# Optimization experiments

Hardware: AMD Instinct MI355X
Metric: run time of the kernel (lower is better)

The kernel has to match this reference:

```python
import jax, jax.numpy as jnp
import numpy as np

H = 128
N_GENE = 100000
N_VAR = 200000
E = 500000


def setup_inputs() -> dict:
    key = jax.random.key(0)
    ks = jax.random.split(key, 24)
    s = 0.05
    inp = {
        "emb_gene": jax.random.normal(ks[0], (N_GENE, H), jnp.float32) * s,
        "emb_var": jax.random.normal(ks[1], (N_VAR, H), jnp.float32) * s,
        "Wl1_gv": jax.random.normal(ks[2], (H, H), jnp.float32) * s,
        "bl1_gv": jnp.zeros((H,), jnp.float32),
        "Wr1_gv": jax.random.normal(ks[3], (H, H), jnp.float32) * s,
        "Wl1_vg": jax.random.normal(ks[4], (H, H), jnp.float32) * s,
        "bl1_vg": jnp.zeros((H,), jnp.float32),
        "Wr1_vg": jax.random.normal(ks[5], (H, H), jnp.float32) * s,
        "Wl2_gv": jax.random.normal(ks[6], (H, H), jnp.float32) * s,
        "bl2_gv": jnp.zeros((H,), jnp.float32),
        "Wr2_gv": jax.random.normal(ks[7], (H, H), jnp.float32) * s,
        "Wl2_vg": jax.random.normal(ks[8], (H, H), jnp.float32) * s,
        "bl2_vg": jnp.zeros((H,), jnp.float32),
        "Wr2_vg": jax.random.normal(ks[9], (H, H), jnp.float32) * s,
        "A1": jax.random.normal(ks[10], (H, H), jnp.float32) * s,
        "b1": jnp.zeros((H,), jnp.float32),
        "A2": jax.random.normal(ks[11], (8, H), jnp.float32) * s,
        "b2": jnp.zeros((8,), jnp.float32),
        "src_gv": jax.random.randint(ks[12], (E,), 0, N_GENE, jnp.int32),
        "dst_gv": jax.random.randint(ks[13], (E,), 0, N_VAR, jnp.int32),
        "src_vg": jax.random.randint(ks[14], (E,), 0, N_VAR, jnp.int32),
        "dst_vg": jax.random.randint(ks[15], (E,), 0, N_GENE, jnp.int32),
    }
    return inp


def _sage(x_src, x_dst, src, dst, Wl, bl, Wr):
    # PyG SAGEConv: lin_l(mean_{j->i} x_src[j]) + lin_r(x_dst[i])
    msg = x_src[src]                                             # [E, H] gather
    agg = jax.ops.segment_sum(msg, dst, num_segments=x_dst.shape[0])
    cnt = jax.ops.segment_sum(jnp.ones_like(src, x_src.dtype), dst,
                              num_segments=x_dst.shape[0])
    mean = agg / jnp.maximum(cnt, 1.0)[:, None]
    return mean @ Wl.T + bl + x_dst @ Wr.T


def reference(emb_gene, emb_var,
              Wl1_gv, bl1_gv, Wr1_gv, Wl1_vg, bl1_vg, Wr1_vg,
              Wl2_gv, bl2_gv, Wr2_gv, Wl2_vg, bl2_vg, Wr2_vg,
              A1, b1, A2, b2,
              src_gv, dst_gv, src_vg, dst_vg):
    # layer 1: gene->variant updates variant; variant->gene updates gene
    h_var = _sage(emb_gene, emb_var, src_gv, dst_gv, Wl1_gv, bl1_gv, Wr1_gv)
    h_gene = _sage(emb_var, emb_gene, src_vg, dst_vg, Wl1_vg, bl1_vg, Wr1_vg)
    z_gene = jax.nn.relu(h_gene)
    z_var = jax.nn.relu(h_var)
    # layer 2
    z_var2 = _sage(z_gene, z_var, src_gv, dst_gv, Wl2_gv, bl2_gv, Wr2_gv)
    z_gene2 = _sage(z_var, z_gene, src_vg, dst_vg, Wl2_vg, bl2_vg, Wr2_vg)
    # adversarial head on 'gene' (GradReverse is identity in forward)
    hdn = jax.nn.relu(z_gene2 @ A1.T + b1)
    adv_gene = hdn @ A2.T + b2
    return (z_gene2, z_var2, adv_gene)
```

## Files before the change

kernel.cpp:

```cpp
#include <hip/hip_runtime.h>
#include <hip/hip_bf16.h>

typedef unsigned short u16;
typedef unsigned int u32;
typedef __attribute__((ext_vector_type(8))) short bf16x8;
typedef __attribute__((ext_vector_type(4))) float f32x4;

#define NG 100000
#define NV 200000
#define NE 500000
#define HD 128
#define NALL (NG + NV)
#define EALL (2 * NE)

__device__ __forceinline__ float bflo(u32 w) { return __uint_as_float(w << 16); }
__device__ __forceinline__ float bfhi(u32 w) { return __uint_as_float(w & 0xffff0000u); }
__device__ __forceinline__ u16 f2bf(float f) {
    __hip_bfloat16 h = __float2bfloat16(f);
    u16 u; __builtin_memcpy(&u, &h, 2); return u;
}
__device__ __forceinline__ u32 pk2(float a, float b) {
    return (u32)f2bf(a) | ((u32)f2bf(b) << 16);
}

__global__ __launch_bounds__(256) void cvt_kernel(const float* __restrict__ g,
                                                  const float* __restrict__ v,
                                                  u16* __restrict__ out) {
    size_t slot = (size_t)blockIdx.x * 256 + threadIdx.x;
    size_t off = slot * 8;
    if (off >= (size_t)NALL * HD) return;
    const float* p = (off < (size_t)NG * HD) ? (g + off) : (v + (off - (size_t)NG * HD));
    float4 a = *(const float4*)p;
    float4 b = *(const float4*)(p + 4);
    uint4 pk;
    pk.x = pk2(a.x, a.y); pk.y = pk2(a.z, a.w);
    pk.z = pk2(b.x, b.y); pk.w = pk2(b.z, b.w);
    *(uint4*)(out + off) = pk;
}

__global__ __launch_bounds__(256) void wcvt_kernel(
    const float* w0, const float* w1, const float* w2, const float* w3,
    const float* w4, const float* w5, const float* w6, const float* w7,
    const float* w8, u16* __restrict__ out)
{
    const float* Ws[9] = {w0, w1, w2, w3, w4, w5, w6, w7, w8};
    const float* W = Ws[blockIdx.x];
    u16* o = out + (size_t)blockIdx.x * 16384;
    int tid = threadIdx.x;
#pragma unroll
    for (int it = 0; it < 8; ++it) {
        int slot = it * 256 + tid;
        int f = slot >> 6, l = slot & 63;
        int kt = f >> 3, ct = f & 7;
        int row = ct * 16 + (l & 15);
        int kof = kt * 32 + (l >> 4) * 8;
        const float* wp = W + (size_t)row * HD + kof;
        float4 x = *(const float4*)wp;
        float4 y = *(const float4*)(wp + 4);
        uint4 pk;
        pk.x = pk2(x.x, x.y); pk.y = pk2(x.z, x.w);
        pk.z = pk2(y.x, y.y); pk.w = pk2(y.z, y.w);
        *(uint4*)(o + (size_t)slot * 8) = pk;
    }
}

__global__ __launch_bounds__(256) void hist2_kernel(const int* __restrict__ dst_gv,
                                                    const int* __restrict__ dst_vg,
                                                    int* __restrict__ deg) {
    int t = blockIdx.x * 256 + threadIdx.x;
    if (t < NE)            atomicAdd(&deg[dst_gv[t]], 1);
    else if (t < EALL)     atomicAdd(&deg[NV + dst_vg[t - NE]], 1);
}

__global__ __launch_bounds__(256) void scan1_kernel(const int* __restrict__ deg,
                                                    int* __restrict__ excl,
                                                    int* __restrict__ bsum, int N) {
    __shared__ int lds[256];
    int tid = threadIdx.x;
    int base = blockIdx.x * 2048 + tid * 8;
    int v[8]; int s = 0;
#pragma unroll
    for (int i = 0; i < 8; ++i) { v[i] = (base + i < N) ? deg[base + i] : 0; s += v[i]; }
    lds[tid] = s;
    __syncthreads();
    for (int off = 1; off < 256; off <<= 1) {
        int x = (tid >= off) ? lds[tid - off] : 0;
        __syncthreads();
        lds[tid] += x;
        __syncthreads();
    }
    int run = lds[tid] - s;
#pragma unroll
    for (int i = 0; i < 8; ++i) {
        if (base + i < N) excl[base + i] = run;
        run += v[i];
    }
    if (tid == 255) bsum[blockIdx.x] = lds[255];
}

__global__ void scan2_kernel(int* __restrict__ bsum, int nb) {
    if (threadIdx.x == 0 && blockIdx.x == 0) {
        int run = 0;
        for (int i = 0; i < nb; ++i) { int t = bsum[i]; bsum[i] = run; run += t; }
    }
}

__global__ __launch_bounds__(256) void scan3_kernel(int* __restrict__ rs,
                                                    int* __restrict__ cur,
                                                    const int* __restrict__ bsum, int N) {
    int i = blockIdx.x * 256 + threadIdx.x;
    if (i < N) {
        int v = rs[i] + bsum[i >> 11];
        rs[i] = v;
        cur[i] = v;
    }
    if (i == 0) rs[N] = EALL;
}

__global__ __launch_bounds__(256) void escatter2_kernel(const int* __restrict__ src_gv,
                                                        const int* __restrict__ dst_gv,
                                                        const int* __restrict__ src_vg,
                                                        const int* __restrict__ dst_vg,
                                                        int* __restrict__ cur,
                                                        int* __restrict__ esrc) {
    int t = blockIdx.x * 256 + threadIdx.x;
    if (t < NE) {
        int p = atomicAdd(&cur[dst_gv[t]], 1);
        esrc[p] = src_gv[t];
    } else if (t < EALL) {
        int e = t - NE;
        int p = atomicAdd(&cur[NV + dst_vg[e]], 1);
        esrc[p] = NG + src_vg[e];
    }
}

template <int RELU, int OBF16>
__global__ __launch_bounds__(256, 4) void fused_sage_kernel(
    const u16* __restrict__ Xb,
    const int* __restrict__ rs,
    const int* __restrict__ esrc,
    const u16* __restrict__ wf_v, const u16* __restrict__ wf_g,
    const float* __restrict__ b_v, const float* __restrict__ b_g,
    float* __restrict__ outf_v, float* __restrict__ outf_g,
    u16* __restrict__ outb_v, u16* __restrict__ outb_g,
    int nvb)
{
    __shared__ __align__(16) char ldsbuf[33792];
    u16* atile = (u16*)ldsbuf;

    const bool isVar = (int)blockIdx.x < nvb;
    const int bseg = isVar ? blockIdx.x : blockIdx.x - nvb;
    const int Nseg = isVar ? NV : NG;
    const int gseg = isVar ? 0 : NV;
    const u16* Xseg = Xb + (size_t)(isVar ? NG : 0) * HD;
    const u16* wf = isVar ? wf_v : wf_g;
    const float* bias = isVar ? b_v : b_g;
    float* outf = isVar ? outf_v : outf_g;
    u16* outb = isVar ? outb_v : outb_g;

    const int tid = threadIdx.x;
    const int lane = tid & 63;
    const int wid = tid >> 6;
    const int m0 = bseg * 128 + wid * 32;
    const int lr = lane & 15, lg = lane >> 4;

    {
        const int c = tid & 15;
        for (int it = 0; it < 8; ++it) {
            int lrow = it * 16 + (tid >> 4);
            int srow = bseg * 128 + lrow;
            float s[8] = {0.f, 0.f, 0.f, 0.f, 0.f, 0.f, 0.f, 0.f};
            float rcv = 0.f;
            if (srow < Nseg) {
                int e0 = rs[gseg + srow], e1 = rs[gseg + srow + 1];
                int e = e0;
                for (; e + 2 <= e1; e += 2) {
                    const u16* p0 = Xb + (size_t)esrc[e] * HD + c * 8;
                    const u16* p1 = Xb + (size_t)esrc[e + 1] * HD + c * 8;
                    uint4 u0 = *(const uint4*)p0;
                    uint4 u1 = *(const uint4*)p1;
                    u32 w0[4] = {u0.x, u0.y, u0.z, u0.w};
                    u32 w1[4] = {u1.x, u1.y, u1.z, u1.w};
#pragma unroll
                    for (int i = 0; i < 4; ++i) {
                        s[2 * i] += bflo(w0[i]) + bflo(w1[i]);
                        s[2 * i + 1] += bfhi(w0[i]) + bfhi(w1[i]);
                    }
                }
                if (e < e1) {
                    const u16* p = Xb + (size_t)esrc[e] * HD + c * 8;
                    uint4 u = *(const uint4*)p;
                    u32 w[4] = {u.x, u.y, u.z, u.w};
#pragma unroll
                    for (int i = 0; i < 4; ++i) { s[2 * i] += bflo(w[i]); s[2 * i + 1] += bfhi(w[i]); }
                }
                rcv = 1.f / fmaxf((float)(e1 - e0), 1.f);
            }
            uint4 pk;
            pk.x = pk2(s[0] * rcv, s[1] * rcv);
            pk.y = pk2(s[2] * rcv, s[3] * rcv);
            pk.z = pk2(s[4] * rcv, s[5] * rcv);
            pk.w = pk2(s[6] * rcv, s[7] * rcv);
            *(uint4*)(atile + lrow * 128 + ((c ^ (lrow & 15)) << 3)) = pk;
        }
    }
    __syncthreads();

    f32x4 acc[2][8];
#pragma unroll
    for (int rt = 0; rt < 2; ++rt)
#pragma unroll
        for (int ct = 0; ct < 8; ++ct) acc[rt][ct] = (f32x4){0.f, 0.f, 0.f, 0.f};

    {
        const u16* wp = wf;
        bf16x8 a[4][2];
#pragma unroll
        for (int kt = 0; kt < 4; ++kt)
#pragma unroll
            for (int rt = 0; rt < 2; ++rt) {
                int lrow = wid * 32 + rt * 16 + lr;
                int ck = (kt * 4 + lg) ^ (lrow & 15);
                a[kt][rt] = *(const bf16x8*)(atile + lrow * 128 + (ck << 3));
            }
#pragma unroll
        for (int kt = 0; kt < 4; ++kt)
#pragma unroll
            for (int ct = 0; ct < 8; ++ct) {
                bf16x8 w = *(const bf16x8*)(wp + (size_t)(((kt * 8 + ct) << 6) + lane) * 8);
#pragma unroll
                for (int rt = 0; rt < 2; ++rt)
                    acc[rt][ct] = __builtin_amdgcn_mfma_f32_16x16x32_bf16(
                        a[kt][rt], w, acc[rt][ct], 0, 0, 0);
            }
    }
    {
        const u16* wp = wf + 16384;
        bf16x8 a[4][2];
#pragma unroll
        for (int kt = 0; kt < 4; ++kt)
#pragma unroll
            for (int rt = 0; rt < 2; ++rt) {
                int row = m0 + rt * 16 + lr; if (row > Nseg - 1) row = Nseg - 1;
                a[kt][rt] = *(const bf16x8*)(Xseg + (size_t)row * HD + kt * 32 + lg * 8);
            }
#pragma unroll
        for (int kt = 0; kt < 4; ++kt)
#pragma unroll
            for (int ct = 0; ct < 8; ++ct) {
                bf16x8 w = *(const bf16x8*)(wp + (size_t)(((kt * 8 + ct) << 6) + lane) * 8);
#pragma unroll
                for (int rt = 0; rt < 2; ++rt)
                    acc[rt][ct] = __builtin_amdgcn_mfma_f32_16x16x32_bf16(
                        a[kt][rt], w, acc[rt][ct], 0, 0, 0);
            }
    }

    float bv[8];
#pragma unroll
    for (int ct = 0; ct < 8; ++ct) bv[ct] = bias[ct * 16 + lr];

    __syncthreads();
    float (*lds_t)[16][132] = (float (*)[16][132])ldsbuf;
#pragma unroll
    for (int rt = 0; rt < 2; ++rt) {
#pragma unroll
        for (int ct = 0; ct < 8; ++ct)
#pragma unroll
            for (int r = 0; r < 4; ++r) {
                float v = acc[rt][ct][r] + bv[ct];
                if (RELU) v = fmaxf(v, 0.f);
                lds_t[wid][lg * 4 + r][ct * 16 + lr] = v;
            }
        __syncthreads();
        if (OBF16 == 0) {
#pragma unroll
            for (int i = 0; i < 8; ++i) {
                int row16 = i * 2 + (lane >> 5);
                int colb = (lane & 31) * 4;
                f32x4 v = *(const f32x4*)&lds_t[wid][row16][colb];
                int grow = m0 + rt * 16 + row16;
                if (grow < Nseg) *(f32x4*)(outf + (size_t)grow * HD + colb) = v;
            }
        } else {
#pragma unroll
            for (int i = 0; i < 4; ++i) {
                int row16 = i * 4 + (lane >> 4);
                int colb = (lane & 15) * 8;
                f32x4 v0 = *(const f32x4*)&lds_t[wid][row16][colb];
                f32x4 v1 = *(const f32x4*)&lds_t[wid][row16][colb + 4];
                uint4 pk;
                pk.x = pk2(v0[0], v0[1]); pk.y = pk2(v0[2], v0[3]);
                pk.z = pk2(v1[0], v1[1]); pk.w = pk2(v1[2], v1[3]);
                int grow = m0 + rt * 16 + row16;
                if (grow < Nseg) *(uint4*)(outb + (size_t)grow * HD + colb) = pk;
            }
        }
        __syncthreads();
    }
}

__global__ __launch_bounds__(256, 4) void head_kernel(
    const float* __restrict__ g2,
    const u16* __restrict__ wfA1,
    const float* __restrict__ b1,
    const float* __restrict__ A2,
    const float* __restrict__ b2,
    float* __restrict__ adv)
{
    __shared__ __align__(16) u16 lds_h[4][16][136];
    const int tid = threadIdx.x;
    const int lane = tid & 63;
    const int wid = tid >> 6;
    const int m0 = blockIdx.x * 128 + wid * 32;
    const int lr = lane & 15, lg = lane >> 4;

    bf16x8 a2f[4];
#pragma unroll
    for (int kt = 0; kt < 4; ++kt) {
        union { u16 s[8]; bf16x8 v; } u;
        if (lr < 8) {
            const float* p = A2 + (size_t)lr * HD + kt * 32 + lg * 8;
            float4 x = *(const float4*)p;
            float4 y = *(const float4*)(p + 4);
            u.s[0] = f2bf(x.x); u.s[1] = f2bf(x.y); u.s[2] = f2bf(x.z); u.s[3] = f2bf(x.w);
            u.s[4] = f2bf(y.x); u.s[5] = f2bf(y.y); u.s[6] = f2bf(y.z); u.s[7] = f2bf(y.w);
        } else {
#pragma unroll
            for (int i = 0; i < 8; ++i) u.s[i] = 0;
        }
        a2f[kt] = u.v;
    }

    f32x4 acc[2][8];
#pragma unroll
    for (int rt = 0; rt < 2; ++rt)
#pragma unroll
        for (int ct = 0; ct < 8; ++ct) acc[rt][ct] = (f32x4){0.f, 0.f, 0.f, 0.f};

#pragma unroll
    for (int kt = 0; kt < 4; ++kt) {
        bf16x8 a[2];
#pragma unroll
        for (int rt = 0; rt < 2; ++rt) {
            int row = m0 + rt * 16 + lr; if (row > NG - 1) row = NG - 1;
            const float* p = g2 + (size_t)row * HD + kt * 32 + lg * 8;
            float4 x = *(const float4*)p;
            float4 y = *(const float4*)(p + 4);
            union { u16 s[8]; bf16x8 v; } u;
            u.s[0] = f2bf(x.x); u.s[1] = f2bf(x.y); u.s[2] = f2bf(x.z); u.s[3] = f2bf(x.w);
            u.s[4] = f2bf(y.x); u.s[5] = f2bf(y.y); u.s[6] = f2bf(y.z); u.s[7] = f2bf(y.w);
            a[rt] = u.v;
        }
#pragma unroll
        for (int ct = 0; ct < 8; ++ct) {
            bf16x8 w = *(const bf16x8*)(wfA1 + (size_t)(((kt * 8 + ct) << 6) + lane) * 8);
#pragma unroll
            for (int rt = 0; rt < 2; ++rt)
                acc[rt][ct] = __builtin_amdgcn_mfma_f32_16x16x32_bf16(
                    a[rt], w, acc[rt][ct], 0, 0, 0);
        }
    }

    float b1v[8];
#pragma unroll
    for (int ct = 0; ct < 8; ++ct) b1v[ct] = b1[ct * 16 + lr];
    float b2v = (lr < 8) ? b2[lr] : 0.f;

#pragma unroll
    for (int rt = 0; rt < 2; ++rt) {
#pragma unroll
        for (int ct = 0; ct < 8; ++ct)
#pragma unroll
            for (int r = 0; r < 4; ++r) {
                float v = fmaxf(acc[rt][ct][r] + b1v[ct], 0.f);
                lds_h[wid][lg * 4 + r][ct * 16 + lr] = f2bf(v);
            }
        __syncthreads();
        f32x4 av = (f32x4){0.f, 0.f, 0.f, 0.f};
#pragma unroll
        for (int kt = 0; kt < 4; ++kt) {
            bf16x8 h = *(const bf16x8*)&lds_h[wid][lr][kt * 32 + lg * 8];
            av = __builtin_amdgcn_mfma_f32_16x16x32_bf16(h, a2f[kt], av, 0, 0, 0);
        }
        if (lr < 8) {
#pragma unroll
            for (int r = 0; r < 4; ++r) {
                int grow = m0 + rt * 16 + lg * 4 + r;
                if (grow < NG) adv[(size_t)grow * 8 + lr] = av[r] + b2v;
            }
        }
        __syncthreads();
    }
}

extern "C" void kernel_launch(void* const* d_in, const int* in_sizes, int n_in,
                              void* d_out, int out_size, void* d_ws, size_t ws_size,
                              hipStream_t stream)
{
    const float* emb_gene = (const float*)d_in[0];
    const float* emb_var  = (const float*)d_in[1];
    const float* Wl1_gv = (const float*)d_in[2];
    const float* bl1_gv = (const float*)d_in[3];
    const float* Wr1_gv = (const float*)d_in[4];
    const float* Wl1_vg = (const float*)d_in[5];
    const float* bl1_vg = (const float*)d_in[6];
    const float* Wr1_vg = (const float*)d_in[7];
    const float* Wl2_gv = (const float*)d_in[8];
    const float* bl2_gv = (const float*)d_in[9];
    const float* Wr2_gv = (const float*)d_in[10];
    const float* Wl2_vg = (const float*)d_in[11];
    const float* bl2_vg = (const float*)d_in[12];
    const float* Wr2_vg = (const float*)d_in[13];
    const float* A1 = (const float*)d_in[14];
    const float* b1 = (const float*)d_in[15];
    const float* A2 = (const float*)d_in[16];
    const float* b2 = (const float*)d_in[17];
    const int* src_gv = (const int*)d_in[18];
    const int* dst_gv = (const int*)d_in[19];
    const int* src_vg = (const int*)d_in[20];
    const int* dst_vg = (const int*)d_in[21];

    char* ws = (char*)d_ws;
    u16* embb  = (u16*)(ws);
    u16* zb    = (u16*)(ws + 76800000);
    u16* wfrag = (u16*)(ws + 153600000);
    int* rs    = (int*)(ws + 154000000);
    int* esrc  = (int*)(ws + 155300000);
    int* deg   = (int*)(ws + 159300000);
    int* cur   = (int*)(ws + 160500000);
    int* bsum  = (int*)(ws + 161700000);

    float* out       = (float*)d_out;
    float* out_gene2 = out;
    float* out_var2  = out + (size_t)NG * HD;
    float* out_adv   = out + (size_t)(NG + NV) * HD;

    const int NB = (NALL + 2047) / 2048;
    const int EB2 = (EALL + 255) / 256;
    const int NVB = (NV + 127) / 128;
    const int NGB = (NG + 127) / 128;
    const int CVB = (int)(((size_t)NALL * HD / 8 + 255) / 256);

    hipMemsetAsync(deg, 0, (size_t)NALL * 4, stream);
    cvt_kernel<<<CVB, 256, 0, stream>>>(emb_gene, emb_var, embb);
    wcvt_kernel<<<9, 256, 0, stream>>>(Wl1_gv, Wr1_gv, Wl1_vg, Wr1_vg,
                                       Wl2_gv, Wr2_gv, Wl2_vg, Wr2_vg, A1, wfrag);
    hist2_kernel<<<EB2, 256, 0, stream>>>(dst_gv, dst_vg, deg);
    scan1_kernel<<<NB, 256, 0, stream>>>(deg, rs, bsum, NALL);
    scan2_kernel<<<1, 64, 0, stream>>>(bsum, NB);
    scan3_kernel<<<(NALL + 255) / 256, 256, 0, stream>>>(rs, cur, bsum, NALL);
    escatter2_kernel<<<EB2, 256, 0, stream>>>(src_gv, dst_gv, src_vg, dst_vg, cur, esrc);

    fused_sage_kernel<1, 1><<<NVB + NGB, 256, 0, stream>>>(embb, rs, esrc,
        wfrag + 0 * 16384, wfrag + 2 * 16384, bl1_gv, bl1_vg,
        nullptr, nullptr,
        zb + (size_t)NG * HD, zb,
        NVB);

    fused_sage_kernel<0, 0><<<NVB + NGB, 256, 0, stream>>>(zb, rs, esrc,
        wfrag + 4 * 16384, wfrag + 6 * 16384, bl2_gv, bl2_vg,
        out_var2, out_gene2,
        nullptr, nullptr,
        NVB);

    head_kernel<<<NGB, 256, 0, stream>>>(out_gene2, wfrag + 8 * 16384, b1, A2, b2, out_adv);
}
```

Measured before the change: 477.3 us.

## Widen gather to four loads in flight, shrink LDS, drop epilogue barriers

The neighbour-gather loop now issues four masked row loads per iteration instead of two, clamping out-of-range indices and zeroing their contribution with a multiplier. This keeps more memory requests in flight to hide gather latency. The epilogue staging moves to per-wave bf16 or half-width fp32 tiles, so LDS fits in 32 KB and launch bounds can ask for 5 blocks per CU. Block-wide barriers are removed where each wave only touches its own LDS slice. The cost is wasted loads on rows whose degree is not a multiple of four, plus extra register pressure.

New measurement: 533.8 us. 1.12x slower.

```diff
diff --git a/kernel.cpp b/kernel.cpp
--- a/kernel.cpp
+++ b/kernel.cpp
@@ -135,7 +135,7 @@
 }
 
 template <int RELU, int OBF16>
-__global__ __launch_bounds__(256, 4) void fused_sage_kernel(
+__global__ __launch_bounds__(256, 5) void fused_sage_kernel(
     const u16* __restrict__ Xb,
     const int* __restrict__ rs,
     const int* __restrict__ esrc,
@@ -145,7 +145,7 @@
     u16* __restrict__ outb_v, u16* __restrict__ outb_g,
     int nvb)
 {
-    __shared__ __align__(16) char ldsbuf[33792];
+    __shared__ __align__(16) char ldsbuf[32768];
     u16* atile = (u16*)ldsbuf;
 
     const bool isVar = (int)blockIdx.x < nvb;
@@ -166,6 +166,7 @@
 
     {
         const int c = tid & 15;
+#pragma unroll 2
         for (int it = 0; it < 8; ++it) {
             int lrow = it * 16 + (tid >> 4);
             int srow = bseg * 128 + lrow;
@@ -173,28 +174,29 @@
             float rcv = 0.f;
             if (srow < Nseg) {
                 int e0 = rs[gseg + srow], e1 = rs[gseg + srow + 1];
-                int e = e0;
-                for (; e + 2 <= e1; e += 2) {
-                    const u16* p0 = Xb + (size_t)esrc[e] * HD + c * 8;
-                    const u16* p1 = Xb + (size_t)esrc[e + 1] * HD + c * 8;
-                    uint4 u0 = *(const uint4*)p0;
-                    uint4 u1 = *(const uint4*)p1;
-                    u32 w0[4] = {u0.x, u0.y, u0.z, u0.w};
-                    u32 w1[4] = {u1.x, u1.y, u1.z, u1.w};
-#pragma unroll
-                    for (int i = 0; i < 4; ++i) {
-                        s[2 * i] += bflo(w0[i]) + bflo(w1[i]);
-                        s[2 * i + 1] += bfhi(w0[i]) + bfhi(w1[i]);
+                if (e1 > e0) {
+                    rcv = 1.f / (float)(e1 - e0);
+                    for (int e = e0; e < e1; e += 4) {
+                        uint4 d[4];
+                        float m[4];
+#pragma unroll
+                        for (int i = 0; i < 4; ++i) {
+                            int ee = e + i;
+                            int idx = esrc[ee < e1 ? ee : e1 - 1];
+                            m[i] = (ee < e1) ? 1.f : 0.f;
+                            d[i] = *(const uint4*)(Xb + (size_t)idx * HD + c * 8);
+                        }
+#pragma unroll
+                        for (int i = 0; i < 4; ++i) {
+                            u32 w[4] = {d[i].x, d[i].y, d[i].z, d[i].w};
+#pragma unroll
+                            for (int j = 0; j < 4; ++j) {
+                                s[2 * j]     = fmaf(m[i], bflo(w[j]), s[2 * j]);
+                                s[2 * j + 1] = fmaf(m[i], bfhi(w[j]), s[2 * j + 1]);
+                            }
+                        }
                     }
                 }
-                if (e < e1) {
-                    const u16* p = Xb + (size_t)esrc[e] * HD + c * 8;
-                    uint4 u = *(const uint4*)p;
-                    u32 w[4] = {u.x, u.y, u.z, u.w};
-#pragma unroll
-                    for (int i = 0; i < 4; ++i) { s[2 * i] += bflo(w[i]); s[2 * i + 1] += bfhi(w[i]); }
-                }
-                rcv = 1.f / fmaxf((float)(e1 - e0), 1.f);
             }
             uint4 pk;
             pk.x = pk2(s[0] * rcv, s[1] * rcv);
@@ -261,42 +263,53 @@
     for (int ct = 0; ct < 8; ++ct) bv[ct] = bias[ct * 16 + lr];
 
     __syncthreads();
-    float (*lds_t)[16][132] = (float (*)[16][132])ldsbuf;
-#pragma unroll
-    for (int rt = 0; rt < 2; ++rt) {
-#pragma unroll
-        for (int ct = 0; ct < 8; ++ct)
-#pragma unroll
-            for (int r = 0; r < 4; ++r) {
-                float v = acc[rt][ct][r] + bv[ct];
-                if (RELU) v = fmaxf(v, 0.f);
-                lds_t[wid][lg * 4 + r][ct * 16 + lr] = v;
-            }
-        __syncthreads();
-        if (OBF16 == 0) {
-#pragma unroll
-            for (int i = 0; i < 8; ++i) {
-                int row16 = i * 2 + (lane >> 5);
-                int colb = (lane & 31) * 4;
-                f32x4 v = *(const f32x4*)&lds_t[wid][row16][colb];
-                int grow = m0 + rt * 16 + row16;
-                if (grow < Nseg) *(f32x4*)(outf + (size_t)grow * HD + colb) = v;
-            }
-        } else {
+    if (OBF16) {
+        u16 (*lds_u)[16][136] = (u16 (*)[16][136])ldsbuf;
+#pragma unroll
+        for (int rt = 0; rt < 2; ++rt) {
+#pragma unroll
+            for (int ct = 0; ct < 8; ++ct)
+#pragma unroll
+                for (int r = 0; r < 4; ++r) {
+                    float v = acc[rt][ct][r] + bv[ct];
+                    if (RELU) v = fmaxf(v, 0.f);
+                    lds_u[wid][lg * 4 + r][ct * 16 + lr] = f2bf(v);
+                }
 #pragma unroll
             for (int i = 0; i < 4; ++i) {
-                int row16 = i * 4 + (lane >> 4);
-                int colb = (lane & 15) * 8;
-                f32x4 v0 = *(const f32x4*)&lds_t[wid][row16][colb];
-                f32x4 v1 = *(const f32x4*)&lds_t[wid][row16][colb + 4];
-                uint4 pk;
-                pk.x = pk2(v0[0], v0[1]); pk.y = pk2(v0[2], v0[3]);
-                pk.z = pk2(v1[0], v1[1]); pk.w = pk2(v1[2], v1[3]);
+                int row16 = i * 4 + lg;
+                int colb = lr * 8;
+                uint4 pk = *(const uint4*)&lds_u[wid][row16][colb];
                 int grow = m0 + rt * 16 + row16;
                 if (grow < Nseg) *(uint4*)(outb + (size_t)grow * HD + colb) = pk;
             }
         }
-        __syncthreads();
+    } else {
+        float (*lds_f)[16][68] = (float (*)[16][68])ldsbuf;
+#pragma unroll
+        for (int rt = 0; rt < 2; ++rt) {
+#pragma unroll
+            for (int p = 0; p < 2; ++p) {
+#pragma unroll
+                for (int cq = 0; cq < 4; ++cq) {
+                    int ct = p * 4 + cq;
+#pragma unroll
+                    for (int r = 0; r < 4; ++r) {
+                        float v = acc[rt][ct][r] + bv[ct];
+                        if (RELU) v = fmaxf(v, 0.f);
+                        lds_f[wid][lg * 4 + r][cq * 16 + lr] = v;
+                    }
+                }
+#pragma unroll
+                for (int i = 0; i < 4; ++i) {
+                    int row16 = i * 4 + lg;
+                    int colb = lr * 4;
+                    f32x4 v = *(const f32x4*)&lds_f[wid][row16][colb];
+                    int grow = m0 + rt * 16 + row16;
+                    if (grow < Nseg) *(f32x4*)(outf + (size_t)grow * HD + p * 64 + colb) = v;
+                }
+            }
+        }
     }
 }
 
@@ -376,7 +389,6 @@
                 float v = fmaxf(acc[rt][ct][r] + b1v[ct], 0.f);
                 lds_h[wid][lg * 4 + r][ct * 16 + lr] = f2bf(v);
             }
-        __syncthreads();
         f32x4 av = (f32x4){0.f, 0.f, 0.f, 0.f};
 #pragma unroll
         for (int kt = 0; kt < 4; ++kt) {
@@ -390,7 +402,6 @@
                 if (grow < NG) adv[(size_t)grow * 8 + lr] = av[r] + b2v;
             }
         }
-        __syncthreads();
     }
 }
 
```
